# Kernel tuning notes

Measured on AMD Instinct MI355X. Metric: run time of the kernel, lower is better.

The kernel has to match this reference:

```python
import jax, jax.numpy as jnp
import numpy as np

BN_EPS = 1e-5
DIST_EPS = 1e-8
K = 3  # fixed 3-NN interpolation


def _cond_conv(x, t_embed, w_t, b_t, w_c, b_c, gamma, beta):
    # time conditioning: GELU(t) -> Linear -> add to channels
    te = jax.nn.gelu(t_embed, approximate=False) @ w_t.T + b_t  # (B, Cin)
    x = x + te[:, :, None]
    # kernel-size-1 Conv1d == channel GEMM
    x = jnp.einsum('oc,bcn->bon', w_c, x) + b_c[None, :, None]
    # BatchNorm1d, training mode: biased stats over (batch, length)
    m = jnp.mean(x, axis=(0, 2), keepdims=True)
    v = jnp.var(x, axis=(0, 2), keepdims=True)
    x = gamma[None, :, None] * (x - m) * jax.lax.rsqrt(v + BN_EPS) + beta[None, :, None]
    return jax.nn.gelu(x, approximate=False)


def _forward(xyz1, xyz2, points1, points2, t_embed,
             w_t1, b_t1, w_c1, b_c1, g1, be1,
             w_t2, b_t2, w_c2, b_c2, g2, be2):
    # squared euclidean distances (cdist**2), computed directly
    # d2[b,n,s] = ||xyz1[b,n]||^2 + ||xyz2[b,s]||^2 - 2 <xyz1[b,n], xyz2[b,s]>
    n1 = jnp.sum(xyz1 * xyz1, axis=-1)  # (B,N)
    n2 = jnp.sum(xyz2 * xyz2, axis=-1)  # (B,S)
    d2 = n1[:, :, None] + n2[:, None, :] - 2.0 * jnp.einsum('bnc,bsc->bns', xyz1, xyz2)
    # top-3 smallest distances (instead of wasteful full sort)
    neg, idx = jax.lax.top_k(-d2, K)        # (B,N,3)
    dists = -neg
    dist_recip = 1.0 / (dists + DIST_EPS)
    weight = dist_recip / jnp.sum(dist_recip, axis=2, keepdims=True)  # (B,N,3)
    pts2t = jnp.transpose(points2, (0, 2, 1))  # (B,S,C2)
    gathered = jax.vmap(lambda p, i: p[i])(pts2t, idx)  # (B,N,3,C2)
    interp = jnp.einsum('bnkc,bnk->bcn', gathered, weight)  # (B,C2,N)
    new_points = jnp.concatenate([points1, interp], axis=1)  # (B,C1+C2,N)
    new_points = _cond_conv(new_points, t_embed, w_t1, b_t1, w_c1, b_c1, g1, be1)
    new_points = _cond_conv(new_points, t_embed, w_t2, b_t2, w_c2, b_c2, g2, be2)
    return new_points


def setup_inputs() -> dict:
    key = jax.random.key(0)
    ks = jax.random.split(key, 12)
    B, N, S, C1, C2, T = 8, 8192, 2048, 128, 256, 256
    Cin = C1 + C2
    s = lambda fan: 1.0 / np.sqrt(fan)
    return {
        'xyz1': jax.random.normal(ks[0], (B, N, 3), jnp.float32),
        'xyz2': jax.random.normal(ks[1], (B, S, 3), jnp.float32),
        'points1': jax.random.normal(ks[2], (B, C1, N), jnp.float32),
        'points2': jax.random.normal(ks[3], (B, C2, S), jnp.float32),
        't_embed': jax.random.normal(ks[4], (B, T), jnp.float32),
        'w_t1': jax.random.normal(ks[5], (Cin, T), jnp.float32) * s(T),
        'b_t1': jnp.zeros((Cin,), jnp.float32),
        'w_c1': jax.random.normal(ks[6], (256, Cin), jnp.float32) * s(Cin),
        'b_c1': jnp.zeros((256,), jnp.float32),
        'g1': jnp.ones((256,), jnp.float32),
        'be1': jnp.zeros((256,), jnp.float32),
        'w_t2': jax.random.normal(ks[7], (256, T), jnp.float32) * s(T),
        'b_t2': jnp.zeros((256,), jnp.float32),
        'w_c2': jax.random.normal(ks[8], (256, 256), jnp.float32) * s(256),
        'b_c2': jnp.zeros((256,), jnp.float32),
        'g2': jnp.ones((256,), jnp.float32),
        'be2': jnp.zeros((256,), jnp.float32),
    }


def reference(xyz1, xyz2, points1, points2, t_embed,
              w_t1, b_t1, w_c1, b_c1, g1, be1,
              w_t2, b_t2, w_c2, b_c2, g2, be2):
    return _forward(xyz1, xyz2, points1, points2, t_embed,
                    w_t1, b_t1, w_c1, b_c1, g1, be1,
                    w_t2, b_t2, w_c2, b_c2, g2, be2)
```

## Files before the change

kernel.cpp:

```cpp
#include <hip/hip_runtime.h>
#include <cfloat>
#include <cmath>

#define B_   8
#define N_   8192
#define S_   2048
#define C1_  128
#define C2_  256
#define T_   256
#define CIN_ 384
#define CO_  256

#define KCH  8
#define KCS  (S_ / KCH)
#define KQB  512

typedef __attribute__((ext_vector_type(8))) short short8;
typedef __attribute__((ext_vector_type(4))) float f32x4;

__device__ __forceinline__ float bf2f(unsigned short u) {
    union { unsigned int i; float f; } v; v.i = ((unsigned int)u) << 16; return v.f;
}
__device__ __forceinline__ unsigned short f2bf(float f) {
    union { float f; unsigned int i; } v; v.f = f;
    unsigned int i = v.i;
    unsigned int r = i + 0x7FFFu + ((i >> 16) & 1u);
    return (unsigned short)(r >> 16);
}
__device__ __forceinline__ float gelu_f(float x) {
    return 0.5f * x * (1.0f + erff(x * 0.70710678118654752440f));
}
__device__ __forceinline__ void async16(const void* g, void* l) {
    __builtin_amdgcn_global_load_lds((const __attribute__((address_space(1))) void*)g,
                                     (__attribute__((address_space(3))) void*)l, 16, 0, 0);
}
__device__ __forceinline__ float med3f(float a, float b, float c) {
    float r;
    asm("v_med3_f32 %0, %1, %2, %3" : "=v"(r) : "v"(a), "v"(b), "v"(c));
    return r;
}

#define OFF_TE1   0u
#define OFF_TE2   16384u
#define OFF_BN1   28672u
#define OFF_BN2   30720u
#define OFF_WC1   1605632u
#define OFF_WC2   1802240u
#define OFF_P2T   2097152u
#define OFF_X1    10485760u
#define OFF_Y     60817408u
#define OFF_PD    OFF_Y
#define OFF_PI    (OFF_Y + 6291456u)
#define OFF_PS    OFF_P2T
#define OFF_PQ    (OFF_P2T + 1048576u)

__global__ __launch_bounds__(256) void mega1_kernel(
    const float* __restrict__ xyz1, const float* __restrict__ xyz2,
    float* __restrict__ pd, int* __restrict__ pi,
    const float* __restrict__ w1, const float* __restrict__ w2,
    unsigned short* __restrict__ o1, unsigned short* __restrict__ o2,
    const float* __restrict__ t_embed,
    const float* __restrict__ w_t1, const float* __restrict__ b_t1,
    const float* __restrict__ w_t2, const float* __restrict__ b_t2,
    float* __restrict__ te1, float* __restrict__ te2,
    const float* __restrict__ p2, unsigned short* __restrict__ p2t)
{
    __shared__ __align__(16) char smem[4096];
    int bx = blockIdx.x, tid = threadIdx.x;

    if (bx < 1024) {
        float4* sp = (float4*)smem;
        int x = bx & 15, ch = (bx >> 4) & 7, b = bx >> 7;
        int s0 = ch * KCS;
        {
            int gs = s0 + tid;
            float xx = xyz2[(b * S_ + gs) * 3 + 0];
            float yy = xyz2[(b * S_ + gs) * 3 + 1];
            float zz = xyz2[(b * S_ + gs) * 3 + 2];
            sp[tid] = make_float4(xx, yy, zz, xx * xx + yy * yy + zz * zz);
        }
        __syncthreads();

        float nx[2], ny[2], nz[2], nn[2];
        float d1[2], d2[2], d3[2];
        int   i1[2], i2[2], i3[2];
        #pragma unroll
        for (int qq = 0; qq < 2; ++qq) {
            int n = x * KQB + qq * 256 + tid;
            float x1 = xyz1[(b * N_ + n) * 3 + 0];
            float y1 = xyz1[(b * N_ + n) * 3 + 1];
            float z1 = xyz1[(b * N_ + n) * 3 + 2];
            nn[qq] = x1 * x1 + y1 * y1 + z1 * z1;
            nx[qq] = -2.0f * x1; ny[qq] = -2.0f * y1; nz[qq] = -2.0f * z1;
            d1[qq] = FLT_MAX; d2[qq] = FLT_MAX; d3[qq] = FLT_MAX;
            i1[qq] = 0; i2[qq] = 0; i3[qq] = 0;
        }

        for (int s = 0; s < KCS; s += 4) {
            #pragma unroll
            for (int u = 0; u < 4; ++u) {
                float4 p = sp[s + u];
                int gi = s0 + s + u;
                #pragma unroll
                for (int qq = 0; qq < 2; ++qq) {
                    float d = fmaf(nx[qq], p.x,
                              fmaf(ny[qq], p.y,
                              fmaf(nz[qq], p.z, p.w)));
                    bool c1 = d < d1[qq];
                    bool c2 = d < d2[qq];
                    bool c3 = d < d3[qq];
                    float e1 = fminf(d1[qq], d);
                    float e2 = med3f(d1[qq], d2[qq], d);
                    float e3 = med3f(d2[qq], d3[qq], d);
                    int u1  = c1 ? i1[qq] : gi;
                    int n1i = c1 ? gi : i1[qq];
                    int n2i = c2 ? u1 : i2[qq];
                    int u2  = c2 ? i2[qq] : gi;
                    int n3i = c3 ? u2 : i3[qq];
                    d1[qq] = e1; d2[qq] = e2; d3[qq] = e3;
                    i1[qq] = n1i; i2[qq] = n2i; i3[qq] = n3i;
                }
            }
        }

        #pragma unroll
        for (int qq = 0; qq < 2; ++qq) {
            int n = x * KQB + qq * 256 + tid;
            size_t pb = (((size_t)b * KCH + ch) * N_ + n) * 3;
            pd[pb + 0] = d1[qq] + nn[qq];
            pd[pb + 1] = d2[qq] + nn[qq];
            pd[pb + 2] = d3[qq] + nn[qq];
            pi[pb + 0] = i1[qq]; pi[pb + 1] = i2[qq]; pi[pb + 2] = i3[qq];
        }
    } else if (bx < 1416) {
        int pbx = bx - 1024;
        if (pbx < 384) {
            int g = pbx * 256 + tid;
            o1[g] = f2bf(w1[g]);
            if (g < CO_ * CO_) o2[g] = f2bf(w2[g]);
            return;
        }
        float* gt = (float*)smem;
        int b = pbx - 384;
        gt[tid] = gelu_f(t_embed[b * T_ + tid]);
        __syncthreads();
        for (int o = tid; o < CIN_ + CO_; o += 256) {
            if (o < CIN_) {
                const float* w = w_t1 + o * T_;
                float s = 0.f;
                for (int k = 0; k < T_; ++k) s += gt[k] * w[k];
                te1[b * CIN_ + o] = s + b_t1[o];
            } else {
                int oo = o - CIN_;
                const float* w = w_t2 + oo * T_;
                float s = 0.f;
                for (int k = 0; k < T_; ++k) s += gt[k] * w[k];
                te2[b * CO_ + oo] = s + b_t2[oo];
            }
        }
    } else {
        unsigned short (*tile)[33] = (unsigned short (*)[33])smem;
        int bz = bx - 1416;
        int b = bz >> 9, cy = (bz >> 6) & 7, sx = bz & 63;
        int s0 = sx * 32, c0 = cy * 32;
        int tx = tid & 31, ty = tid >> 5;
        #pragma unroll
        for (int j = 0; j < 4; ++j) {
            int c = ty + j * 8;
            tile[c][tx] = f2bf(p2[((size_t)b * C2_ + c0 + c) * S_ + s0 + tx]);
        }
        __syncthreads();
        #pragma unroll
        for (int j = 0; j < 4; ++j) {
            int s = ty + j * 8;
            p2t[((size_t)b * S_ + s0 + s) * C2_ + c0 + tx] = tile[tx][s];
        }
    }
}

__global__ __launch_bounds__(256) void mega2_kernel(
    const float* __restrict__ pd, const int* __restrict__ pi,
    const unsigned short* __restrict__ p2t,
    const float* __restrict__ te1,
    const float* __restrict__ p1,
    unsigned short* __restrict__ X1)
{
    __shared__ __align__(16) char smem[4096];
    int bx = blockIdx.x, tid = threadIdx.x;

    if (bx < 8192) {
        float (*spd)[8][3] = (float (*)[8][3])smem;
        int   (*spi)[8][3] = (int (*)[8][3])(smem + 768);
        float* ste = (float*)(smem + 1536);
        int b = bx >> 10;
        int n0 = (bx & 1023) * 8;
        ste[tid] = te1[b * CIN_ + C1_ + tid];
        if (tid < 64) {
            int ch = tid >> 3, r = tid & 7;
            size_t pb = (((size_t)b * KCH + ch) * N_ + n0 + r) * 3;
            spd[ch][r][0] = pd[pb]; spd[ch][r][1] = pd[pb + 1]; spd[ch][r][2] = pd[pb + 2];
        } else if (tid < 128) {
            int t2 = tid - 64;
            int ch = t2 >> 3, r = t2 & 7;
            size_t pb = (((size_t)b * KCH + ch) * N_ + n0 + r) * 3;
            spi[ch][r][0] = pi[pb]; spi[ch][r][1] = pi[pb + 1]; spi[ch][r][2] = pi[pb + 2];
        }
        __syncthreads();

        int r = tid >> 5;
        int l = tid & 31;
        float d1, d2, d3; int i1, i2, i3;
        if (l < KCH) {
            d1 = spd[l][r][0]; d2 = spd[l][r][1]; d3 = spd[l][r][2];
            i1 = spi[l][r][0]; i2 = spi[l][r][1]; i3 = spi[l][r][2];
        } else {
            d1 = d2 = d3 = FLT_MAX;
            i1 = i2 = i3 = 0x7FFFFFFF;
        }
        #pragma unroll
        for (int m = 1; m <= 4; m <<= 1) {
            float pd1 = __shfl_xor(d1, m), pd2 = __shfl_xor(d2, m), pd3 = __shfl_xor(d3, m);
            int   pi1 = __shfl_xor(i1, m), pi2 = __shfl_xor(i2, m), pi3 = __shfl_xor(i3, m);
            #pragma unroll
            for (int k = 0; k < 3; ++k) {
                float d = (k == 0) ? pd1 : (k == 1) ? pd2 : pd3;
                int   i = (k == 0) ? pi1 : (k == 1) ? pi2 : pi3;
                bool c1 = (d < d1) || (d == d1 && i < i1);
                bool c2 = (d < d2) || (d == d2 && i < i2);
                bool c3 = (d < d3) || (d == d3 && i < i3);
                float e1 = c1 ? d : d1;        int j1 = c1 ? i : i1;
                float e2 = c1 ? d1 : (c2 ? d : d2);
                int   j2 = c1 ? i1 : (c2 ? i : i2);
                float e3 = c2 ? d2 : (c3 ? d : d3);
                int   j3 = c2 ? i2 : (c3 ? i : i3);
                d1 = e1; d2 = e2; d3 = e3; i1 = j1; i2 = j2; i3 = j3;
            }
        }
        int base = tid & 32;
        d1 = __shfl(d1, base); d2 = __shfl(d2, base); d3 = __shfl(d3, base);
        i1 = __shfl(i1, base); i2 = __shfl(i2, base); i3 = __shfl(i3, base);
        float r1 = 1.0f / (d1 + 1e-8f);
        float r2 = 1.0f / (d2 + 1e-8f);
        float r3 = 1.0f / (d3 + 1e-8f);
        float rs = 1.0f / (r1 + r2 + r3);
        float w0 = r1 * rs, w1 = r2 * rs, w2 = r3 * rs;

        int gr = (b << 13) + n0 + r;
        int co = l * 8;
        const unsigned short* q0 = p2t + ((size_t)b * S_ + i1) * C2_ + co;
        const unsigned short* q1 = p2t + ((size_t)b * S_ + i2) * C2_ + co;
        const unsigned short* q2 = p2t + ((size_t)b * S_ + i3) * C2_ + co;
        union { short8 v; unsigned short u[8]; } a0, a1, a2, pk;
        a0.v = *(const short8*)q0;
        a1.v = *(const short8*)q1;
        a2.v = *(const short8*)q2;
        #pragma unroll
        for (int jj = 0; jj < 8; ++jj) {
            float v = w0 * bf2f(a0.u[jj]) + w1 * bf2f(a1.u[jj]) + w2 * bf2f(a2.u[jj])
                    + ste[co + jj];
            pk.u[jj] = f2bf(v);
        }
        *(short8*)&X1[(size_t)gr * CIN_ + C1_ + co] = pk.v;
    } else {
        unsigned short (*tile)[33] = (unsigned short (*)[33])smem;
        int bz = bx - 8192;
        int b = bz >> 10, cy = (bz >> 8) & 3, nx = bz & 255;
        int n0 = nx * 32, c0 = cy * 32;
        int tx = tid & 31, ty = tid >> 5;
        const float* te = te1 + b * CIN_;
        #pragma unroll
        for (int j = 0; j < 4; ++j) {
            int c = ty + j * 8;
            tile[c][tx] =
                f2bf(p1[((size_t)b * C1_ + c0 + c) * N_ + n0 + tx] + te[c0 + c]);
        }
        __syncthreads();
        #pragma unroll
        for (int j = 0; j < 4; ++j) {
            int n = ty + j * 8;
            X1[((size_t)b * N_ + n0 + n) * CIN_ + c0 + tx] = tile[tx][n];
        }
    }
}

template <int K, int MODE>
__global__ __launch_bounds__(256) void gemm_bt(
    const unsigned short* __restrict__ A,
    const unsigned short* __restrict__ X,
    const float* __restrict__ bias,
    unsigned short* __restrict__ out,
    float* __restrict__ psum, float* __restrict__ psq)
{
    __shared__ unsigned short sA[128 * 64];
    __shared__ unsigned short sB[128 * 64];
    const int tid = threadIdx.x;
    const int lane = tid & 63, wave = tid >> 6;
    const int wo = wave >> 1, wm = wave & 1;
    const int quad = lane >> 4, col = lane & 15;
    const int b = blockIdx.z;
    const int x = blockIdx.x;
    const int perm = (x & 7) * 16 + (x >> 3);
    const int n_t = perm >> 1, o_t = perm & 1;
    const int o0 = o_t * 128;
    const int n0 = n_t * 128;
    const unsigned short* Xb = X + (size_t)b * N_ * K;
    const int prow = ((b << 6) + n_t) * 2 + wm;

    f32x4 acc[4][4];
    #pragma unroll
    for (int i = 0; i < 4; ++i)
        #pragma unroll
        for (int j = 0; j < 4; ++j) acc[i][j] = (f32x4){0.f, 0.f, 0.f, 0.f};

    for (int k0 = 0; k0 < K; k0 += 64) {
        #pragma unroll
        for (int i = 0; i < 4; ++i) {
            int chunk = i * 256 + tid;
            int row = chunk >> 3, c8 = chunk & 7;
            async16(&A [(o0 + row) * K + k0 + c8 * 8], &sA[chunk * 8]);
            async16(&Xb[(size_t)(n0 + row) * K + k0 + c8 * 8], &sB[chunk * 8]);
        }
        __syncthreads();
        #pragma unroll
        for (int kk = 0; kk < 64; kk += 32) {
            short8 af[4], bfr[4];
            #pragma unroll
            for (int i = 0; i < 4; ++i)
                af[i] = *(const short8*)&sA[(wo * 64 + i * 16 + col) * 64 + kk + quad * 8];
            #pragma unroll
            for (int j = 0; j < 4; ++j)
                bfr[j] = *(const short8*)&sB[(wm * 64 + j * 16 + col) * 64 + kk + quad * 8];
            #pragma unroll
            for (int i = 0; i < 4; ++i)
                #pragma unroll
                for (int j = 0; j < 4; ++j)
                    acc[i][j] = __builtin_amdgcn_mfma_f32_16x16x32_bf16(af[i], bfr[j], acc[i][j], 0, 0, 0);
        }
        __syncthreads();
    }

    #pragma unroll
    for (int i = 0; i < 4; ++i) {
        int oo = o0 + wo * 64 + i * 16 + quad * 4;
        float bv0 = bias[oo + 0], bv1 = bias[oo + 1];
        float bv2 = bias[oo + 2], bv3 = bias[oo + 3];
        float s0 = 0.f, s1 = 0.f, s2 = 0.f, s3 = 0.f;
        float q0 = 0.f, q1 = 0.f, q2 = 0.f, q3 = 0.f;
        #pragma unroll
        for (int j = 0; j < 4; ++j) {
            int nn = n0 + wm * 64 + j * 16 + col;
            float v0 = acc[i][j][0] + bv0, v1 = acc[i][j][1] + bv1;
            float v2 = acc[i][j][2] + bv2, v3 = acc[i][j][3] + bv3;
            s0 += v0; q0 += v0 * v0; s1 += v1; q1 += v1 * v1;
            s2 += v2; q2 += v2 * v2; s3 += v3; q3 += v3 * v3;
            if (MODE == 0) {
                union { unsigned short u[4]; uint2 p; } pk;
                pk.u[0] = f2bf(v0); pk.u[1] = f2bf(v1);
                pk.u[2] = f2bf(v2); pk.u[3] = f2bf(v3);
                *(uint2*)&out[((size_t)b * N_ + nn) * CO_ + oo] = pk.p;
            } else {
                out[((size_t)b * CO_ + oo + 0) * N_ + nn] = f2bf(v0);
                out[((size_t)b * CO_ + oo + 1) * N_ + nn] = f2bf(v1);
                out[((size_t)b * CO_ + oo + 2) * N_ + nn] = f2bf(v2);
                out[((size_t)b * CO_ + oo + 3) * N_ + nn] = f2bf(v3);
            }
        }
        #pragma unroll
        for (int off = 1; off < 16; off <<= 1) {
            s0 += __shfl_down(s0, off); q0 += __shfl_down(q0, off);
            s1 += __shfl_down(s1, off); q1 += __shfl_down(q1, off);
            s2 += __shfl_down(s2, off); q2 += __shfl_down(q2, off);
            s3 += __shfl_down(s3, off); q3 += __shfl_down(q3, off);
        }
        if (col == 0) {
            float* ps = psum + (size_t)oo * 1024 + prow;
            float* pq = psq  + (size_t)oo * 1024 + prow;
            ps[0] = s0; ps[1024] = s1; ps[2048] = s2; ps[3072] = s3;
            pq[0] = q0; pq[1024] = q1; pq[2048] = q2; pq[3072] = q3;
        }
    }
}

__global__ __launch_bounds__(256) void bn_reduce_kernel(
    const float* __restrict__ psum, const float* __restrict__ psq,
    const float* __restrict__ gamma, const float* __restrict__ beta,
    float* __restrict__ scale, float* __restrict__ shift)
{
    int ch = blockIdx.x * 8 + (threadIdx.x >> 5);
    int l = threadIdx.x & 31;
    float s = 0.f, q = 0.f;
    for (int r = l; r < 1024; r += 32) {
        s += psum[(size_t)ch * 1024 + r];
        q += psq [(size_t)ch * 1024 + r];
    }
    #pragma unroll
    for (int off = 16; off > 0; off >>= 1) {
        s += __shfl_down(s, off, 32);
        q += __shfl_down(q, off, 32);
    }
    if (l == 0) {
        const float inv = 1.0f / 65536.0f;
        float m = s * inv;
        float var = fmaxf(q * inv - m * m, 0.f);
        float sc = gamma[ch] / sqrtf(var + 1e-5f);
        scale[ch] = sc;
        shift[ch] = beta[ch] - m * sc;
    }
}

__global__ __launch_bounds__(256) void apply1_kernel(
    unsigned short* __restrict__ y, const float* __restrict__ scale,
    const float* __restrict__ shift, const float* __restrict__ te2)
{
    __shared__ float ssc[CO_], ssh[CO_], ste[CO_];
    int b = blockIdx.x >> 10;
    int t = threadIdx.x;
    ssc[t] = scale[t]; ssh[t] = shift[t]; ste[t] = te2[b * CO_ + t];
    __syncthreads();
    int g = blockIdx.x * 256 + t;
    int row = g >> 5;
    int og = (g & 31) * 8;
    unsigned short* p = y + (size_t)row * CO_ + og;
    union { short8 v; unsigned short u[8]; } in, op;
    in.v = *(short8*)p;
    #pragma unroll
    for (int jj = 0; jj < 8; ++jj) {
        int o = og + jj;
        op.u[jj] = f2bf(gelu_f(ssc[o] * bf2f(in.u[jj]) + ssh[o]) + ste[o]);
    }
    *(short8*)p = op.v;
}

__global__ __launch_bounds__(256) void final_kernel(
    const unsigned short* __restrict__ z, const float* __restrict__ scale,
    const float* __restrict__ shift, float* __restrict__ out)
{
    int g = blockIdx.x * 256 + threadIdx.x;
    size_t e = (size_t)g * 8;
    int row = (int)(e >> 13);
    int o = row & (CO_ - 1);
    float sc = scale[o], sh = shift[o];
    union { short8 v; unsigned short u[8]; } in;
    in.v = *(const short8*)&z[e];
    float vo[8];
    #pragma unroll
    for (int jj = 0; jj < 8; ++jj)
        vo[jj] = gelu_f(sc * bf2f(in.u[jj]) + sh);
    *(float4*)&out[e]     = make_float4(vo[0], vo[1], vo[2], vo[3]);
    *(float4*)&out[e + 4] = make_float4(vo[4], vo[5], vo[6], vo[7]);
}

extern "C" void kernel_launch(void* const* d_in, const int* in_sizes, int n_in,
                              void* d_out, int out_size, void* d_ws, size_t ws_size,
                              hipStream_t stream)
{
    (void)in_sizes; (void)n_in; (void)out_size; (void)ws_size;
    const float* xyz1    = (const float*)d_in[0];
    const float* xyz2    = (const float*)d_in[1];
    const float* points1 = (const float*)d_in[2];
    const float* points2 = (const float*)d_in[3];
    const float* t_embed = (const float*)d_in[4];
    const float* w_t1    = (const float*)d_in[5];
    const float* b_t1    = (const float*)d_in[6];
    const float* w_c1    = (const float*)d_in[7];
    const float* b_c1    = (const float*)d_in[8];
    const float* g1      = (const float*)d_in[9];
    const float* be1     = (const float*)d_in[10];
    const float* w_t2    = (const float*)d_in[11];
    const float* b_t2    = (const float*)d_in[12];
    const float* w_c2    = (const float*)d_in[13];
    const float* b_c2    = (const float*)d_in[14];
    const float* g2      = (const float*)d_in[15];
    const float* be2     = (const float*)d_in[16];

    char* w = (char*)d_ws;
    float* te1        = (float*)(w + OFF_TE1);
    float* te2        = (float*)(w + OFF_TE2);
    float* scale1     = (float*)(w + OFF_BN1);
    float* shift1     = scale1 + 256;
    float* scale2     = (float*)(w + OFF_BN2);
    float* shift2     = scale2 + 256;
    unsigned short* wc1 = (unsigned short*)(w + OFF_WC1);
    unsigned short* wc2 = (unsigned short*)(w + OFF_WC2);
    unsigned short* p2t = (unsigned short*)(w + OFF_P2T);
    float* pd         = (float*)(w + OFF_PD);
    int*   pi         = (int*)(w + OFF_PI);
    float* psum       = (float*)(w + OFF_PS);
    float* psq        = (float*)(w + OFF_PQ);
    unsigned short* X1  = (unsigned short*)(w + OFF_X1);
    unsigned short* Z   = (unsigned short*)(w + OFF_X1);
    unsigned short* Y   = (unsigned short*)(w + OFF_Y);
    float* out = (float*)d_out;

    hipLaunchKernelGGL(mega1_kernel, dim3(5512), dim3(256), 0, stream,
                       xyz1, xyz2, pd, pi,
                       w_c1, w_c2, wc1, wc2,
                       t_embed, w_t1, b_t1, w_t2, b_t2, te1, te2,
                       points2, p2t);
    hipLaunchKernelGGL(mega2_kernel, dim3(16384), dim3(256), 0, stream,
                       pd, pi, p2t, te1, points1, X1);
    hipLaunchKernelGGL((gemm_bt<CIN_, 0>), dim3(128, 1, B_), dim3(256), 0, stream,
                       wc1, X1, b_c1, Y, psum, psq);
    hipLaunchKernelGGL(bn_reduce_kernel, dim3(32), dim3(256), 0, stream,
                       psum, psq, g1, be1, scale1, shift1);
    hipLaunchKernelGGL(apply1_kernel, dim3(8192), dim3(256), 0, stream,
                       Y, scale1, shift1, te2);
    hipLaunchKernelGGL((gemm_bt<CO_, 1>), dim3(128, 1, B_), dim3(256), 0, stream,
                       wc2, Y, b_c2, Z, psum, psq);
    hipLaunchKernelGGL(bn_reduce_kernel, dim3(32), dim3(256), 0, stream,
                       psum, psq, g2, be2, scale2, shift2);
    hipLaunchKernelGGL(final_kernel, dim3(8192), dim3(256), 0, stream,
                       Z, scale2, shift2, out);
}
```

Baseline: 319.0 us.

## Fold time-embedding add into per-batch conv bias and move points1 transpose

Uses linearity W(x+te) = Wx + W·te to precompute a per-batch bias (b_c + W_c·te) in the small time-conditioning blocks, so the te1/te2 additions are removed from the interpolation, transpose and apply1 elementwise paths. The GEMMs now read a per-batch bias vector. The points1 transpose blocks move from mega2 into mega1, which grows mega1's grid and leaves mega2 doing only the interpolation. The bias matvec runs in only 8 blocks with serial 384-long loops, which could become a tail in mega1. Adding te after bf16 rounding is also no longer needed.

```diff
diff --git a/kernel.cpp b/kernel.cpp
--- a/kernel.cpp
+++ b/kernel.cpp
@@ -40,8 +40,8 @@
     return r;
 }
 
-#define OFF_TE1   0u
-#define OFF_TE2   16384u
+#define OFF_B1    0u
+#define OFF_B2    8192u
 #define OFF_BN1   28672u
 #define OFF_BN2   30720u
 #define OFF_WC1   1605632u
@@ -62,8 +62,10 @@
     const float* __restrict__ t_embed,
     const float* __restrict__ w_t1, const float* __restrict__ b_t1,
     const float* __restrict__ w_t2, const float* __restrict__ b_t2,
-    float* __restrict__ te1, float* __restrict__ te2,
-    const float* __restrict__ p2, unsigned short* __restrict__ p2t)
+    const float* __restrict__ b_c1, const float* __restrict__ b_c2,
+    float* __restrict__ bias1, float* __restrict__ bias2,
+    const float* __restrict__ p2, unsigned short* __restrict__ p2t,
+    const float* __restrict__ p1, unsigned short* __restrict__ X1)
 {
     __shared__ __align__(16) char smem[4096];
     int bx = blockIdx.x, tid = threadIdx.x;
@@ -132,16 +134,15 @@
             pd[pb + 2] = d3[qq] + nn[qq];
             pi[pb + 0] = i1[qq]; pi[pb + 1] = i2[qq]; pi[pb + 2] = i3[qq];
         }
+    } else if (bx < 1408) {
+        int g = (bx - 1024) * 256 + tid;
+        o1[g] = f2bf(w1[g]);
+        if (g < CO_ * CO_) o2[g] = f2bf(w2[g]);
     } else if (bx < 1416) {
-        int pbx = bx - 1024;
-        if (pbx < 384) {
-            int g = pbx * 256 + tid;
-            o1[g] = f2bf(w1[g]);
-            if (g < CO_ * CO_) o2[g] = f2bf(w2[g]);
-            return;
-        }
-        float* gt = (float*)smem;
-        int b = pbx - 384;
+        float* gt   = (float*)smem;
+        float* te1s = gt + T_;
+        float* te2s = te1s + CIN_;
+        int b = bx - 1408;
         gt[tid] = gelu_f(t_embed[b * T_ + tid]);
         __syncthreads();
         for (int o = tid; o < CIN_ + CO_; o += 256) {
@@ -149,16 +150,28 @@
                 const float* w = w_t1 + o * T_;
                 float s = 0.f;
                 for (int k = 0; k < T_; ++k) s += gt[k] * w[k];
-                te1[b * CIN_ + o] = s + b_t1[o];
+                te1s[o] = s + b_t1[o];
             } else {
                 int oo = o - CIN_;
                 const float* w = w_t2 + oo * T_;
                 float s = 0.f;
                 for (int k = 0; k < T_; ++k) s += gt[k] * w[k];
-                te2[b * CO_ + oo] = s + b_t2[oo];
+                te2s[oo] = s + b_t2[oo];
             }
         }
-    } else {
+        __syncthreads();
+        {
+            int o = tid;
+            const float* wr1 = w1 + (size_t)o * CIN_;
+            float s1 = b_c1[o];
+            for (int c = 0; c < CIN_; ++c) s1 += wr1[c] * te1s[c];
+            bias1[b * CO_ + o] = s1;
+            const float* wr2 = w2 + (size_t)o * CO_;
+            float s2 = b_c2[o];
+            for (int c = 0; c < CO_; ++c) s2 += wr2[c] * te2s[c];
+            bias2[b * CO_ + o] = s2;
+        }
+    } else if (bx < 5512) {
         unsigned short (*tile)[33] = (unsigned short (*)[33])smem;
         int bz = bx - 1416;
         int b = bz >> 9, cy = (bz >> 6) & 7, sx = bz & 63;
@@ -175,112 +188,101 @@
             int s = ty + j * 8;
             p2t[((size_t)b * S_ + s0 + s) * C2_ + c0 + tx] = tile[tx][s];
         }
+    } else {
+        unsigned short (*tile)[33] = (unsigned short (*)[33])smem;
+        int bz = bx - 5512;
+        int b = bz >> 10, cy = (bz >> 8) & 3, nx = bz & 255;
+        int n0 = nx * 32, c0 = cy * 32;
+        int tx = tid & 31, ty = tid >> 5;
+        #pragma unroll
+        for (int j = 0; j < 4; ++j) {
+            int c = ty + j * 8;
+            tile[c][tx] = f2bf(p1[((size_t)b * C1_ + c0 + c) * N_ + n0 + tx]);
+        }
+        __syncthreads();
+        #pragma unroll
+        for (int j = 0; j < 4; ++j) {
+            int n = ty + j * 8;
+            X1[((size_t)b * N_ + n0 + n) * CIN_ + c0 + tx] = tile[tx][n];
+        }
     }
 }
 
 __global__ __launch_bounds__(256) void mega2_kernel(
     const float* __restrict__ pd, const int* __restrict__ pi,
     const unsigned short* __restrict__ p2t,
-    const float* __restrict__ te1,
-    const float* __restrict__ p1,
     unsigned short* __restrict__ X1)
 {
-    __shared__ __align__(16) char smem[4096];
-    int bx = blockIdx.x, tid = threadIdx.x;
-
-    if (bx < 8192) {
-        float (*spd)[8][3] = (float (*)[8][3])smem;
-        int   (*spi)[8][3] = (int (*)[8][3])(smem + 768);
-        float* ste = (float*)(smem + 1536);
-        int b = bx >> 10;
-        int n0 = (bx & 1023) * 8;
-        ste[tid] = te1[b * CIN_ + C1_ + tid];
-        if (tid < 64) {
-            int ch = tid >> 3, r = tid & 7;
-            size_t pb = (((size_t)b * KCH + ch) * N_ + n0 + r) * 3;
-            spd[ch][r][0] = pd[pb]; spd[ch][r][1] = pd[pb + 1]; spd[ch][r][2] = pd[pb + 2];
-        } else if (tid < 128) {
-            int t2 = tid - 64;
-            int ch = t2 >> 3, r = t2 & 7;
-            size_t pb = (((size_t)b * KCH + ch) * N_ + n0 + r) * 3;
-            spi[ch][r][0] = pi[pb]; spi[ch][r][1] = pi[pb + 1]; spi[ch][r][2] = pi[pb + 2];
-        }
-        __syncthreads();
-
-        int r = tid >> 5;
-        int l = tid & 31;
-        float d1, d2, d3; int i1, i2, i3;
-        if (l < KCH) {
-            d1 = spd[l][r][0]; d2 = spd[l][r][1]; d3 = spd[l][r][2];
-            i1 = spi[l][r][0]; i2 = spi[l][r][1]; i3 = spi[l][r][2];
-        } else {
-            d1 = d2 = d3 = FLT_MAX;
-            i1 = i2 = i3 = 0x7FFFFFFF;
-        }
-        #pragma unroll
-        for (int m = 1; m <= 4; m <<= 1) {
-            float pd1 = __shfl_xor(d1, m), pd2 = __shfl_xor(d2, m), pd3 = __shfl_xor(d3, m);
-            int   pi1 = __shfl_xor(i1, m), pi2 = __shfl_xor(i2, m), pi3 = __shfl_xor(i3, m);
-            #pragma unroll
-            for (int k = 0; k < 3; ++k) {
-                float d = (k == 0) ? pd1 : (k == 1) ? pd2 : pd3;
-                int   i = (k == 0) ? pi1 : (k == 1) ? pi2 : pi3;
-                bool c1 = (d < d1) || (d == d1 && i < i1);
-                bool c2 = (d < d2) || (d == d2 && i < i2);
-                bool c3 = (d < d3) || (d == d3 && i < i3);
-                float e1 = c1 ? d : d1;        int j1 = c1 ? i : i1;
-                float e2 = c1 ? d1 : (c2 ? d : d2);
-                int   j2 = c1 ? i1 : (c2 ? i : i2);
-                float e3 = c2 ? d2 : (c3 ? d : d3);
-                int   j3 = c2 ? i2 : (c3 ? i : i3);
-                d1 = e1; d2 = e2; d3 = e3; i1 = j1; i2 = j2; i3 = j3;
-            }
-        }
-        int base = tid & 32;
-        d1 = __shfl(d1, base); d2 = __shfl(d2, base); d3 = __shfl(d3, base);
-        i1 = __shfl(i1, base); i2 = __shfl(i2, base); i3 = __shfl(i3, base);
-        float r1 = 1.0f / (d1 + 1e-8f);
-        float r2 = 1.0f / (d2 + 1e-8f);
-        float r3 = 1.0f / (d3 + 1e-8f);
-        float rs = 1.0f / (r1 + r2 + r3);
-        float w0 = r1 * rs, w1 = r2 * rs, w2 = r3 * rs;
-
-        int gr = (b << 13) + n0 + r;
-        int co = l * 8;
-        const unsigned short* q0 = p2t + ((size_t)b * S_ + i1) * C2_ + co;
-        const unsigned short* q1 = p2t + ((size_t)b * S_ + i2) * C2_ + co;
-        const unsigned short* q2 = p2t + ((size_t)b * S_ + i3) * C2_ + co;
-        union { short8 v; unsigned short u[8]; } a0, a1, a2, pk;
-        a0.v = *(const short8*)q0;
-        a1.v = *(const short8*)q1;
-        a2.v = *(const short8*)q2;
-        #pragma unroll
-        for (int jj = 0; jj < 8; ++jj) {
-            float v = w0 * bf2f(a0.u[jj]) + w1 * bf2f(a1.u[jj]) + w2 * bf2f(a2.u[jj])
-                    + ste[co + jj];
-            pk.u[jj] = f2bf(v);
-        }
-        *(short8*)&X1[(size_t)gr * CIN_ + C1_ + co] = pk.v;
+    __shared__ float spd[KCH][8][3];
+    __shared__ int   spi[KCH][8][3];
+    int tid = threadIdx.x;
+    int b = blockIdx.x >> 10;
+    int n0 = (blockIdx.x & 1023) * 8;
+    if (tid < 64) {
+        int ch = tid >> 3, r = tid & 7;
+        size_t pb = (((size_t)b * KCH + ch) * N_ + n0 + r) * 3;
+        spd[ch][r][0] = pd[pb]; spd[ch][r][1] = pd[pb + 1]; spd[ch][r][2] = pd[pb + 2];
+    } else if (tid < 128) {
+        int t2 = tid - 64;
+        int ch = t2 >> 3, r = t2 & 7;
+        size_t pb = (((size_t)b * KCH + ch) * N_ + n0 + r) * 3;
+        spi[ch][r][0] = pi[pb]; spi[ch][r][1] = pi[pb + 1]; spi[ch][r][2] = pi[pb + 2];
+    }
+    __syncthreads();
+
+    int r = tid >> 5;
+    int l = tid & 31;
+    float d1, d2, d3; int i1, i2, i3;
+    if (l < KCH) {
+        d1 = spd[l][r][0]; d2 = spd[l][r][1]; d3 = spd[l][r][2];
+        i1 = spi[l][r][0]; i2 = spi[l][r][1]; i3 = spi[l][r][2];
     } else {
-        unsigned short (*tile)[33] = (unsigned short (*)[33])smem;
-        int bz = bx - 8192;
-        int b = bz >> 10, cy = (bz >> 8) & 3, nx = bz & 255;
-        int n0 = nx * 32, c0 = cy * 32;
-        int tx = tid & 31, ty = tid >> 5;
-        const float* te = te1 + b * CIN_;
-        #pragma unroll
-        for (int j = 0; j < 4; ++j) {
-            int c = ty + j * 8;
-            tile[c][tx] =
-                f2bf(p1[((size_t)b * C1_ + c0 + c) * N_ + n0 + tx] + te[c0 + c]);
-        }
-        __syncthreads();
-        #pragma unroll
-        for (int j = 0; j < 4; ++j) {
-            int n = ty + j * 8;
-            X1[((size_t)b * N_ + n0 + n) * CIN_ + c0 + tx] = tile[tx][n];
-        }
-    }
+        d1 = d2 = d3 = FLT_MAX;
+        i1 = i2 = i3 = 0x7FFFFFFF;
+    }
+    #pragma unroll
+    for (int m = 1; m <= 4; m <<= 1) {
+        float pd1 = __shfl_xor(d1, m), pd2 = __shfl_xor(d2, m), pd3 = __shfl_xor(d3, m);
+        int   pi1 = __shfl_xor(i1, m), pi2 = __shfl_xor(i2, m), pi3 = __shfl_xor(i3, m);
+        #pragma unroll
+        for (int k = 0; k < 3; ++k) {
+            float d = (k == 0) ? pd1 : (k == 1) ? pd2 : pd3;
+            int   i = (k == 0) ? pi1 : (k == 1) ? pi2 : pi3;
+            bool c1 = (d < d1) || (d == d1 && i < i1);
+            bool c2 = (d < d2) || (d == d2 && i < i2);
+            bool c3 = (d < d3) || (d == d3 && i < i3);
+            float e1 = c1 ? d : d1;        int j1 = c1 ? i : i1;
+            float e2 = c1 ? d1 : (c2 ? d : d2);
+            int   j2 = c1 ? i1 : (c2 ? i : i2);
+            float e3 = c2 ? d2 : (c3 ? d : d3);
+            int   j3 = c2 ? i2 : (c3 ? i : i3);
+            d1 = e1; d2 = e2; d3 = e3; i1 = j1; i2 = j2; i3 = j3;
+        }
+    }
+    int base = tid & 32;
+    d1 = __shfl(d1, base); d2 = __shfl(d2, base); d3 = __shfl(d3, base);
+    i1 = __shfl(i1, base); i2 = __shfl(i2, base); i3 = __shfl(i3, base);
+    float r1 = 1.0f / (d1 + 1e-8f);
+    float r2 = 1.0f / (d2 + 1e-8f);
+    float r3 = 1.0f / (d3 + 1e-8f);
+    float rs = 1.0f / (r1 + r2 + r3);
+    float w0 = r1 * rs, w1 = r2 * rs, w2 = r3 * rs;
+
+    int gr = (b << 13) + n0 + r;
+    int co = l * 8;
+    const unsigned short* q0 = p2t + ((size_t)b * S_ + i1) * C2_ + co;
+    const unsigned short* q1 = p2t + ((size_t)b * S_ + i2) * C2_ + co;
+    const unsigned short* q2 = p2t + ((size_t)b * S_ + i3) * C2_ + co;
+    union { short8 v; unsigned short u[8]; } a0, a1, a2, pk;
+    a0.v = *(const short8*)q0;
+    a1.v = *(const short8*)q1;
+    a2.v = *(const short8*)q2;
+    #pragma unroll
+    for (int jj = 0; jj < 8; ++jj) {
+        float v = w0 * bf2f(a0.u[jj]) + w1 * bf2f(a1.u[jj]) + w2 * bf2f(a2.u[jj]);
+        pk.u[jj] = f2bf(v);
+    }
+    *(short8*)&X1[(size_t)gr * CIN_ + C1_ + co] = pk.v;
 }
 
 template <int K, int MODE>
@@ -304,6 +306,7 @@
     const int o0 = o_t * 128;
     const int n0 = n_t * 128;
     const unsigned short* Xb = X + (size_t)b * N_ * K;
+    const float* bias_b = bias + b * CO_;
     const int prow = ((b << 6) + n_t) * 2 + wm;
 
     f32x4 acc[4][4];
@@ -342,8 +345,8 @@
     #pragma unroll
     for (int i = 0; i < 4; ++i) {
         int oo = o0 + wo * 64 + i * 16 + quad * 4;
-        float bv0 = bias[oo + 0], bv1 = bias[oo + 1];
-        float bv2 = bias[oo + 2], bv3 = bias[oo + 3];
+        float bv0 = bias_b[oo + 0], bv1 = bias_b[oo + 1];
+        float bv2 = bias_b[oo + 2], bv3 = bias_b[oo + 3];
         float s0 = 0.f, s1 = 0.f, s2 = 0.f, s3 = 0.f;
         float q0 = 0.f, q1 = 0.f, q2 = 0.f, q3 = 0.f;
         #pragma unroll
@@ -410,12 +413,11 @@
 
 __global__ __launch_bounds__(256) void apply1_kernel(
     unsigned short* __restrict__ y, const float* __restrict__ scale,
-    const float* __restrict__ shift, const float* __restrict__ te2)
-{
-    __shared__ float ssc[CO_], ssh[CO_], ste[CO_];
-    int b = blockIdx.x >> 10;
+    const float* __restrict__ shift)
+{
+    __shared__ float ssc[CO_], ssh[CO_];
     int t = threadIdx.x;
-    ssc[t] = scale[t]; ssh[t] = shift[t]; ste[t] = te2[b * CO_ + t];
+    ssc[t] = scale[t]; ssh[t] = shift[t];
     __syncthreads();
     int g = blockIdx.x * 256 + t;
     int row = g >> 5;
@@ -426,7 +428,7 @@
     #pragma unroll
     for (int jj = 0; jj < 8; ++jj) {
         int o = og + jj;
-        op.u[jj] = f2bf(gelu_f(ssc[o] * bf2f(in.u[jj]) + ssh[o]) + ste[o]);
+        op.u[jj] = f2bf(gelu_f(ssc[o] * bf2f(in.u[jj]) + ssh[o]));
     }
     *(short8*)p = op.v;
 }
@@ -474,8 +476,8 @@
     const float* be2     = (const float*)d_in[16];
 
     char* w = (char*)d_ws;
-    float* te1        = (float*)(w + OFF_TE1);
-    float* te2        = (float*)(w + OFF_TE2);
+    float* bias1      = (float*)(w + OFF_B1);
+    float* bias2      = (float*)(w + OFF_B2);
     float* scale1     = (float*)(w + OFF_BN1);
     float* shift1     = scale1 + 256;
     float* scale2     = (float*)(w + OFF_BN2);
@@ -492,21 +494,22 @@
     unsigned short* Y   = (unsigned short*)(w + OFF_Y);
     float* out = (float*)d_out;
 
-    hipLaunchKernelGGL(mega1_kernel, dim3(5512), dim3(256), 0, stream,
+    hipLaunchKernelGGL(mega1_kernel, dim3(13704), dim3(256), 0, stream,
                        xyz1, xyz2, pd, pi,
                        w_c1, w_c2, wc1, wc2,
-                       t_embed, w_t1, b_t1, w_t2, b_t2, te1, te2,
-                       points2, p2t);
-    hipLaunchKernelGGL(mega2_kernel, dim3(16384), dim3(256), 0, stream,
-                       pd, pi, p2t, te1, points1, X1);
+                       t_embed, w_t1, b_t1, w_t2, b_t2,
+                       b_c1, b_c2, bias1, bias2,
+                       points2, p2t, points1, X1);
+    hipLaunchKernelGGL(mega2_kernel, dim3(8192), dim3(256), 0, stream,
+                       pd, pi, p2t, X1);
     hipLaunchKernelGGL((gemm_bt<CIN_, 0>), dim3(128, 1, B_), dim3(256), 0, stream,
-                       wc1, X1, b_c1, Y, psum, psq);
+                       wc1, X1, bias1, Y, psum, psq);
     hipLaunchKernelGGL(bn_reduce_kernel, dim3(32), dim3(256), 0, stream,
                        psum, psq, g1, be1, scale1, shift1);
     hipLaunchKernelGGL(apply1_kernel, dim3(8192), dim3(256), 0, stream,
-                       Y, scale1, shift1, te2);
+                       Y, scale1, shift1);
     hipLaunchKernelGGL((gemm_bt<CO_, 1>), dim3(128, 1, B_), dim3(256), 0, stream,
-                       wc2, Y, b_c2, Z, psum, psq);
+                       wc2, Y, bias2, Z, psum, psq);
     hipLaunchKernelGGL(bn_reduce_kernel, dim3(32), dim3(256), 0, stream,
                        psum, psq, g2, be2, scale2, shift2);
     hipLaunchKernelGGL(final_kernel, dim3(8192), dim3(256), 0, stream,
```

After: 319.3 us. About the same (+0.1%).
